# Optimization experiments

Measured on AMD Instinct MI355X. Metric: run time of the kernel, lower is better.

Reference implementation:

```python
import jax, jax.numpy as jnp
import numpy as np

N, T, M, D, H, FD, FF, L, B = 24, 120, 3, 32, 2, 16, 64, 3, 64
SCALE = 1.0 / np.sqrt(FD)  # torch MHA scales q by 1/sqrt(head_dim)
NEG = -1e9


def _make_pe():
    # Faithful to the module's (nonstandard) encoding: denominator uses 2*i/D for every i.
    t = np.arange(T, dtype=np.float64)[:, None]
    i = np.arange(D, dtype=np.float64)[None, :]
    denom = np.power(10000.0, 2.0 * i / D)
    pe = np.where(i % 2 == 0, np.sin(t / denom), np.cos(t / denom))
    return jnp.asarray(pe, jnp.float32)  # (T, D)


def _ln(x, g, b):
    mu = x.mean(-1, keepdims=True)
    var = x.var(-1, keepdims=True)
    return (x - mu) / jnp.sqrt(var + 1e-5) * g + b


def setup_inputs() -> dict:
    key = jax.random.key(0)
    keys = iter(jax.random.split(key, 48))
    def nrm(shape, s=0.1):
        return jax.random.normal(next(keys), shape, jnp.float32) * s
    inp = {
        'X': jax.random.normal(next(keys), (B, T, N * M), jnp.float32),
        'pe': _make_pe(),
        'E_W': nrm((N, M, D)), 'E_b': nrm((N, D), 0.01),
        'tq_W': nrm((N, D, D)), 'tq_b': nrm((N, D), 0.01),
        'tk_W': nrm((N, D, D)), 'tk_b': nrm((N, D), 0.01),
        'tv_W': nrm((N, D, D)), 'tv_b': nrm((N, D), 0.01),
        'tm_Wq': nrm((N, D, D)), 'tm_bq': nrm((N, D), 0.01),
        'tm_Wk': nrm((N, D, D)), 'tm_bk': nrm((N, D), 0.01),
        'tm_Wv': nrm((N, D, D)), 'tm_bv': nrm((N, D), 0.01),
        'tm_Wo': nrm((N, D, D)), 'tm_bo': nrm((N, D), 0.01),
        'sq_W': nrm((T, D, D)), 'sq_b': nrm((T, D), 0.01),
        'sk_W': nrm((T, D, D)), 'sk_b': nrm((T, D), 0.01),
        'sv_W': nrm((T, D, D)), 'sv_b': nrm((T, D), 0.01),
        'sm_Wq': nrm((T, D, D)), 'sm_bq': nrm((T, D), 0.01),
        'sm_Wk': nrm((T, D, D)), 'sm_bk': nrm((T, D), 0.01),
        'sm_Wv': nrm((T, D, D)), 'sm_bv': nrm((T, D), 0.01),
        'sm_Wo': nrm((T, D, D)), 'sm_bo': nrm((T, D), 0.01),
        'ff1_W': nrm((D, FF)), 'ff1_b': nrm((FF,), 0.01),
        'ff2_W': nrm((FF, D)), 'ff2_b': nrm((D,), 0.01),
        'ln_g': jnp.ones((D,), jnp.float32), 'ln_b': jnp.zeros((D,), jnp.float32),
        'op_W': nrm((N, D, M)), 'op_b': nrm((N, M), 0.01),
    }
    return inp


def reference(X, pe, E_W, E_b, tq_W, tq_b, tk_W, tk_b, tv_W, tv_b,
              tm_Wq, tm_bq, tm_Wk, tm_bk, tm_Wv, tm_bv, tm_Wo, tm_bo,
              sq_W, sq_b, sk_W, sk_b, sv_W, sv_b,
              sm_Wq, sm_bq, sm_Wk, sm_bk, sm_Wv, sm_bv, sm_Wo, sm_bo,
              ff1_W, ff1_b, ff2_W, ff2_b, ln_g, ln_b, op_W, op_b):
    b = X.shape[0]
    Xr = X.reshape(b, T, N, M)
    # per-joint embedding + positional encoding (dropout = identity in eval)
    E = jnp.einsum('btnm,nmd->btnd', Xr, E_W) + E_b + pe[None, :, None, :]
    causal = jnp.triu(jnp.full((T, T), NEG, jnp.float32), 1)
    for _ in range(L):
        # ---- temporal attention: per node n, causal over time ----
        q = jnp.einsum('btnd,nde->btne', E, tq_W) + tq_b
        k = jnp.einsum('btnd,nde->btne', E, tk_W) + tk_b
        v = jnp.einsum('btnd,nde->btne', E, tv_W) + tv_b
        qp = (jnp.einsum('btnd,nde->btne', q, tm_Wq) + tm_bq).reshape(b, T, N, H, FD)
        kp = (jnp.einsum('btnd,nde->btne', k, tm_Wk) + tm_bk).reshape(b, T, N, H, FD)
        vp = (jnp.einsum('btnd,nde->btne', v, tm_Wv) + tm_bv).reshape(b, T, N, H, FD)
        scores = jnp.einsum('bqnhf,bknhf->bnhqk', qp, kp) * SCALE + causal
        attn = jax.nn.softmax(scores, axis=-1)
        o = jnp.einsum('bnhqk,bknhf->bqnhf', attn, vp).reshape(b, T, N, D)
        t_sum = jnp.einsum('btnd,nde->btne', o, tm_Wo) + tm_bo
        t_norm = _ln(E + t_sum, ln_g, ln_b)
        # ---- spatial attention: per timestep t, full over nodes ----
        q = jnp.einsum('btnd,tde->btne', E, sq_W) + sq_b[:, None]
        k = jnp.einsum('btnd,tde->btne', E, sk_W) + sk_b[:, None]
        v = jnp.einsum('btnd,tde->btne', E, sv_W) + sv_b[:, None]
        qp = (jnp.einsum('btnd,tde->btne', q, sm_Wq) + sm_bq[:, None]).reshape(b, T, N, H, FD)
        kp = (jnp.einsum('btnd,tde->btne', k, sm_Wk) + sm_bk[:, None]).reshape(b, T, N, H, FD)
        vp = (jnp.einsum('btnd,tde->btne', v, sm_Wv) + sm_bv[:, None]).reshape(b, T, N, H, FD)
        scores = jnp.einsum('btqhf,btkhf->bthqk', qp, kp) * SCALE
        attn = jax.nn.softmax(scores, axis=-1)
        o = jnp.einsum('bthqk,btkhf->btqhf', attn, vp).reshape(b, T, N, D)
        s_sum = jnp.einsum('btnd,tde->btne', o, sm_Wo) + sm_bo[:, None]
        s_norm = _ln(E + s_sum, ln_g, ln_b)
        # ---- shared feedforward + norm ----
        ts = t_norm + s_norm
        ff = jax.nn.relu(ts @ ff1_W + ff1_b) @ ff2_W + ff2_b
        E = _ln(ff + ts, ln_g, ln_b)
    out = jnp.einsum('btnd,ndm->btnm', E, op_W) + op_b
    return out.reshape(b, T, N * M) + X
```

## Files before the change

kernel.cpp:

```cpp
#include <hip/hip_runtime.h>
#include <hip/hip_bf16.h>

typedef __hip_bfloat16 bf16;
typedef __fp16 h2 __attribute__((ext_vector_type(2)));
typedef _Float16 f16x2 __attribute__((ext_vector_type(2)));

constexpr int B  = 64, T = 120, N = 24, M = 3, D = 32;
constexpr int NH = 2, FD = 16, FF = 64, L = 3;
constexpr float SCALE = 0.25f;
constexpr int SK  = 40;
constexpr int SOH = 20;
constexpr int CH2 = 30;
constexpr int NJ  = 30;
constexpr int QR  = 64;
constexpr int QCH = (B * T) / QR;
constexpr int QEH = 20;
constexpr int BG  = 2;
constexpr int SR  = N * BG;
constexpr int SEH = 20;
constexpr int FR  = 32;

__device__ __forceinline__ float b2f(bf16 x) { return __bfloat162float(x); }
__device__ __forceinline__ float blo(unsigned u) { return __uint_as_float(u << 16); }
__device__ __forceinline__ float bhi(unsigned u) { return __uint_as_float(u & 0xffff0000u); }
__device__ __forceinline__ unsigned pk2(float a, float b) {
  bf16 x = __float2bfloat16(a), y = __float2bfloat16(b);
  unsigned short ux = *reinterpret_cast<unsigned short*>(&x);
  unsigned short uy = *reinterpret_cast<unsigned short*>(&y);
  return (unsigned)ux | ((unsigned)uy << 16);
}
__device__ __forceinline__ unsigned pkh2(float a, float b) {
  h2 r = __builtin_amdgcn_cvt_pkrtz(a, b);
  return *reinterpret_cast<unsigned*>(&r);
}
__device__ __forceinline__ h2 u2h(unsigned u) { return *reinterpret_cast<h2*>(&u); }
__device__ __forceinline__ f16x2 u2f(unsigned u) { return *reinterpret_cast<f16x2*>(&u); }

__global__ __launch_bounds__(256) void compose3_kernel(
    const float* __restrict__ W1q, const float* __restrict__ b1q,
    const float* __restrict__ W2q, const float* __restrict__ b2q,
    const float* __restrict__ W1k, const float* __restrict__ b1k,
    const float* __restrict__ W2k, const float* __restrict__ b2k,
    const float* __restrict__ W1v, const float* __restrict__ b1v,
    const float* __restrict__ W2v, const float* __restrict__ b2v,
    float* __restrict__ Wc, float* __restrict__ bc, int U) {
  int fam = blockIdx.x / U;
  int n   = blockIdx.x % U;
  const float* W1 = (fam == 0) ? W1q : (fam == 1) ? W1k : W1v;
  const float* b1 = (fam == 0) ? b1q : (fam == 1) ? b1k : b1v;
  const float* W2 = (fam == 0) ? W2q : (fam == 1) ? W2k : W2v;
  const float* b2 = (fam == 0) ? b2q : (fam == 1) ? b2k : b2v;
  const float* w1 = W1 + n * D * D;
  const float* w2 = W2 + n * D * D;
  float* wc  = Wc + (size_t)(fam * U + n) * D * D;
  float* bcp = bc + (fam * U + n) * D;
  __shared__ float s1[D * D], s2[D * D];
  for (int i = threadIdx.x; i < D * D; i += 256) { s1[i] = w1[i]; s2[i] = w2[i]; }
  __syncthreads();
  for (int i = threadIdx.x; i < D * D; i += 256) {
    int d = i >> 5, f = i & 31;
    float acc = 0.f;
#pragma unroll
    for (int e = 0; e < D; ++e) acc += s1[d * D + e] * s2[e * D + f];
    wc[i] = acc;
  }
  if (threadIdx.x < D) {
    int f = threadIdx.x;
    float acc = b2[n * D + f];
#pragma unroll
    for (int e = 0; e < D; ++e) acc += b1[n * D + e] * s2[e * D + f];
    bcp[f] = acc;
  }
}

__global__ __launch_bounds__(256) void embed_kernel(
    const float* __restrict__ X, const float* __restrict__ pe,
    const float* __restrict__ E_W, const float* __restrict__ E_b,
    bf16* __restrict__ E) {
  int idx = blockIdx.x * 256 + threadIdx.x;
  if (idx >= B * T * N * D) return;
  int d = idx & 31;
  int n = (idx >> 5) % N;
  int bt = idx / (D * N);
  int t = bt % T;
  const float* x = X + bt * (N * M) + n * M;
  float acc = E_b[n * D + d] + pe[t * D + d];
#pragma unroll
  for (int m = 0; m < M; ++m) acc += x[m] * E_W[(n * M + m) * D + d];
  E[idx] = __float2bfloat16(acc);
}

__global__ __launch_bounds__(256) void qkvt_kernel(
    const bf16* __restrict__ E, const float* __restrict__ WtC,
    const float* __restrict__ btC,
    bf16* __restrict__ Qt, bf16* __restrict__ Kt, bf16* __restrict__ Vt) {
  int n     = blockIdx.x / QCH;
  int chunk = blockIdx.x % QCH;
  __shared__ unsigned whh[3 * (D / 2) * D];
  __shared__ float bsh[3 * D];
  __shared__ __align__(16) unsigned Esp[QR * QEH];
  int tid = threadIdx.x;
  for (int i = tid; i < 3 * (D / 2) * D; i += 256) {
    int fam = i / ((D / 2) * D);
    int idx = i % ((D / 2) * D);
    int d2 = idx >> 5, j = idx & 31;
    const float* wg = WtC + (size_t)(fam * N + n) * D * D;
    whh[i] = pkh2(wg[(2 * d2) * D + j], wg[(2 * d2 + 1) * D + j]);
  }
  if (tid < 3 * D) {
    int fam = tid >> 5, e = tid & 31;
    bsh[tid] = btC[(fam * N + n) * D + e];
  }
  {
    int row = tid >> 2, p = tid & 3;
    const bf16* er = E + ((size_t)(chunk * QR + row) * N + n) * D;
    uint4 u = *(const uint4*)&er[p * 8];
    uint4 o;
    o.x = pkh2(blo(u.x), bhi(u.x));
    o.y = pkh2(blo(u.y), bhi(u.y));
    o.z = pkh2(blo(u.z), bhi(u.z));
    o.w = pkh2(blo(u.w), bhi(u.w));
    *(uint4*)&Esp[row * QEH + p * 4] = o;
  }
  __syncthreads();

  int row = tid >> 2, q = tid & 3;
  int grow = chunk * QR + row;
  int b = grow / T, t = grow % T;
  unsigned xp[D / 2];
#pragma unroll
  for (int d2 = 0; d2 < D / 2; ++d2) xp[d2] = Esp[row * QEH + d2];
  size_t dsto = (((size_t)b * N + n) * T + t) * D + q * 8;
  bf16* dsts[3] = { Qt + dsto, Kt + dsto, Vt + dsto };
#pragma unroll
  for (int fam = 0; fam < 3; ++fam) {
    const unsigned* wf = whh + fam * (D / 2) * D;
    const float* bi = bsh + fam * D;
    float a[8];
#pragma unroll
    for (int j = 0; j < 8; ++j) a[j] = bi[q * 8 + j];
#pragma unroll
    for (int d2 = 0; d2 < D / 2; ++d2) {
      h2 x = u2h(xp[d2]);
#pragma unroll
      for (int j = 0; j < 8; ++j)
        a[j] = __builtin_amdgcn_fdot2(x, u2h(wf[d2 * D + q * 8 + j]), a[j], false);
    }
    uint4 o;
    o.x = pk2(a[0], a[1]); o.y = pk2(a[2], a[3]);
    o.z = pk2(a[4], a[5]); o.w = pk2(a[6], a[7]);
    *(uint4*)dsts[fam] = o;
  }
}

__global__ __launch_bounds__(256) void attnt_kernel(
    const bf16* __restrict__ Qt, const bf16* __restrict__ Kt,
    const bf16* __restrict__ Vt, const bf16* __restrict__ E,
    const float* __restrict__ tm_Wo, const float* __restrict__ tm_bo,
    const float* __restrict__ ln_g, const float* __restrict__ ln_b,
    bf16* __restrict__ Tn) {
  int bn = blockIdx.x;
  int n  = bn % N, b = bn / N;
  __shared__ __align__(16) __fp16 Klh[T * SK];
  __shared__ __align__(16) __fp16 Vlh[T * SK];
  __shared__ __align__(16) __fp16 Qlh[CH2 * SK];
  __shared__ __align__(16) unsigned Olh[CH2 * SOH];
  __shared__ unsigned woh[(D / 2) * D];
  __shared__ float bol[D], gl[D], bbl[D];
  int tid = threadIdx.x;

  const bf16* Kg = Kt + (size_t)bn * T * D;
  const bf16* Vg = Vt + (size_t)bn * T * D;
  const bf16* Qg = Qt + (size_t)bn * T * D;
  for (int i = tid; i < T * 4; i += 256) {
    int r = i >> 2, p = i & 3;
    uint4 ku = *(const uint4*)&Kg[r * D + p * 8];
    uint4 kh;
    kh.x = pkh2(blo(ku.x), bhi(ku.x));
    kh.y = pkh2(blo(ku.y), bhi(ku.y));
    kh.z = pkh2(blo(ku.z), bhi(ku.z));
    kh.w = pkh2(blo(ku.w), bhi(ku.w));
    *(uint4*)&Klh[r * SK + p * 8] = kh;
    uint4 vu = *(const uint4*)&Vg[r * D + p * 8];
    uint4 vh;
    vh.x = pkh2(blo(vu.x), bhi(vu.x));
    vh.y = pkh2(blo(vu.y), bhi(vu.y));
    vh.z = pkh2(blo(vu.z), bhi(vu.z));
    vh.w = pkh2(blo(vu.w), bhi(vu.w));
    *(uint4*)&Vlh[r * SK + p * 8] = vh;
  }
  {
    const float* wg = tm_Wo + (size_t)n * D * D;
    for (int i = tid; i < (D / 2) * D; i += 256) {
      int d2 = i >> 5, e = i & 31;
      woh[i] = pkh2(wg[(2 * d2) * D + e], wg[(2 * d2 + 1) * D + e]);
    }
  }
  if (tid < D) {
    bol[tid] = tm_bo[n * D + tid];
    gl[tid]  = ln_g[tid];
    bbl[tid] = ln_b[tid];
  }
  __syncthreads();

#pragma unroll
  for (int c = 0; c < 4; ++c) {
    const int JM = (CH2 * (c + 1) + 3) >> 2;
    if (tid < CH2 * 4) {
      int r = tid >> 2, p = tid & 3;
      uint4 qu = *(const uint4*)&Qg[(CH2 * c + r) * D + p * 8];
      uint4 qh;
      qh.x = pkh2(blo(qu.x), bhi(qu.x));
      qh.y = pkh2(blo(qu.y), bhi(qu.y));
      qh.z = pkh2(blo(qu.z), bhi(qu.z));
      qh.w = pkh2(blo(qu.w), bhi(qu.w));
      *(uint4*)&Qlh[r * SK + p * 8] = qh;
    }
    __syncthreads();

    {
      int task = tid >> 2, sl = tid & 3;
      if (task < 2 * CH2) {
        int rl = task >> 1, h = task & 1, ho = h * FD;
        int rg = CH2 * c + rl;
        uint4 q0 = *(const uint4*)&Qlh[rl * SK + ho];
        uint4 q1 = *(const uint4*)&Qlh[rl * SK + ho + 8];
        unsigned qh[8] = { q0.x, q0.y, q0.z, q0.w, q1.x, q1.y, q1.z, q1.w };

        float sc[NJ];
        float mx = -3e38f;
#pragma unroll
        for (int j = 0; j < JM; ++j) {
          int k = 4 * j + sl;
          sc[j] = -3e38f;
          if (k <= rg) {
            const uint4 ka = *(const uint4*)&Klh[k * SK + ho];
            const uint4 kb = *(const uint4*)&Klh[k * SK + ho + 8];
            float s0 = __builtin_amdgcn_fdot2(u2h(qh[0]), u2h(ka.x), 0.f, false);
            float s1 = __builtin_amdgcn_fdot2(u2h(qh[1]), u2h(ka.y), 0.f, false);
            float s2 = __builtin_amdgcn_fdot2(u2h(qh[2]), u2h(ka.z), 0.f, false);
            float s3 = __builtin_amdgcn_fdot2(u2h(qh[3]), u2h(ka.w), 0.f, false);
            s0 = __builtin_amdgcn_fdot2(u2h(qh[4]), u2h(kb.x), s0, false);
            s1 = __builtin_amdgcn_fdot2(u2h(qh[5]), u2h(kb.y), s1, false);
            s2 = __builtin_amdgcn_fdot2(u2h(qh[6]), u2h(kb.z), s2, false);
            s3 = __builtin_amdgcn_fdot2(u2h(qh[7]), u2h(kb.w), s3, false);
            float s = ((s0 + s1) + (s2 + s3)) * SCALE;
            sc[j] = s;
            mx = fmaxf(mx, s);
          }
        }
        mx = fmaxf(mx, __shfl_xor(mx, 1, 64));
        mx = fmaxf(mx, __shfl_xor(mx, 2, 64));
        float l = 0.f;
#pragma unroll
        for (int j = 0; j < JM; ++j) {
          sc[j] = __expf(sc[j] - mx);
          l += sc[j];
        }
        l += __shfl_xor(l, 1, 64);
        l += __shfl_xor(l, 2, 64);
        float rli = 1.f / l;

        f16x2 acc2[8];
#pragma unroll
        for (int f = 0; f < 8; ++f) acc2[f] = f16x2{(_Float16)0.f, (_Float16)0.f};
#pragma unroll
        for (int j = 0; j < JM; ++j) {
          int k = 4 * j + sl;
          if (k <= rg) {
            f16x2 pp = f16x2{(_Float16)sc[j], (_Float16)sc[j]};
            const uint4 va = *(const uint4*)&Vlh[k * SK + ho];
            const uint4 vb = *(const uint4*)&Vlh[k * SK + ho + 8];
            acc2[0] += pp * u2f(va.x);
            acc2[1] += pp * u2f(va.y);
            acc2[2] += pp * u2f(va.z);
            acc2[3] += pp * u2f(va.w);
            acc2[4] += pp * u2f(vb.x);
            acc2[5] += pp * u2f(vb.y);
            acc2[6] += pp * u2f(vb.z);
            acc2[7] += pp * u2f(vb.w);
          }
        }
#pragma unroll
        for (int f = 0; f < 8; ++f) {
          unsigned u = *reinterpret_cast<unsigned*>(&acc2[f]);
          unsigned u1 = __shfl_xor(u, 1, 64);
          acc2[f] += u2f(u1);
          u = *reinterpret_cast<unsigned*>(&acc2[f]);
          unsigned u2_ = __shfl_xor(u, 2, 64);
          acc2[f] += u2f(u2_);
        }
        if (sl == 0) {
#pragma unroll
          for (int j = 0; j < 8; ++j)
            Olh[rl * SOH + h * 8 + j] =
                pkh2((float)acc2[j][0] * rli, (float)acc2[j][1] * rli);
        }
      }
    }
    __syncthreads();

    {
      int rl = tid >> 3, q = tid & 7, e0 = q * 4;
      if (rl < CH2) {
        int rg = CH2 * c + rl;
        size_t rowo = ((size_t)(b * T + rg) * N + n) * D;
        uint2 eu = *(const uint2*)&E[rowo + e0];
        float res[4] = { blo(eu.x), bhi(eu.x), blo(eu.y), bhi(eu.y) };
        float o[4], s1 = 0.f, s2 = 0.f;
#pragma unroll
        for (int j = 0; j < 4; ++j) {
          int e = e0 + j;
          float a = bol[e] + res[j];
#pragma unroll
          for (int d2 = 0; d2 < D / 2; ++d2)
            a = __builtin_amdgcn_fdot2(u2h(Olh[rl * SOH + d2]),
                                       u2h(woh[d2 * D + e]), a, false);
          o[j] = a; s1 += a; s2 += a * a;
        }
        s1 += __shfl_xor(s1, 1, 64); s2 += __shfl_xor(s2, 1, 64);
        s1 += __shfl_xor(s1, 2, 64); s2 += __shfl_xor(s2, 2, 64);
        s1 += __shfl_xor(s1, 4, 64); s2 += __shfl_xor(s2, 4, 64);
        float mu  = s1 * (1.f / D);
        float var = s2 * (1.f / D) - mu * mu;
        float r = rsqrtf(var + 1e-5f);
        uint2 ou;
        ou.x = pk2((o[0]-mu)*r*gl[e0]+bbl[e0],    (o[1]-mu)*r*gl[e0+1]+bbl[e0+1]);
        ou.y = pk2((o[2]-mu)*r*gl[e0+2]+bbl[e0+2],(o[3]-mu)*r*gl[e0+3]+bbl[e0+3]);
        *(uint2*)&Tn[rowo + e0] = ou;
      }
    }
  }
}

__global__ __launch_bounds__(256) void spatial_kernel(
    const bf16* __restrict__ E, const float* __restrict__ WsC,
    const float* __restrict__ bsC, const float* __restrict__ sm_Wo,
    const float* __restrict__ sm_bo, const float* __restrict__ ln_g,
    const float* __restrict__ ln_b, bf16* __restrict__ Sn) {
  int t  = blockIdx.x >> 5;
  int bg = blockIdx.x & 31;
  int b0 = bg * BG;
  __shared__ unsigned Wh[3 * (D / 2) * D];
  __shared__ unsigned woh[(D / 2) * D];
  __shared__ float bqs[D], bks[D], bvs[D], bos[D], gs[D], bbs[D];
  __shared__ __align__(16) unsigned Esh[SR * SEH];
  __shared__ __align__(16) __fp16 Qh[SR * SK];
  __shared__ __align__(16) __fp16 Kh[SR * SK];
  __shared__ __align__(16) __fp16 Vh[SR * SK];
  int tid = threadIdx.x;

  for (int i = tid; i < 3 * (D / 2) * D; i += 256) {
    int fam = i / ((D / 2) * D);
    int idx = i % ((D / 2) * D);
    int d2 = idx >> 5, e = idx & 31;
    const float* wg = WsC + (size_t)(fam * T + t) * D * D;
    Wh[i] = pkh2(wg[(2 * d2) * D + e], wg[(2 * d2 + 1) * D + e]);
  }
  {
    const float* wg = sm_Wo + (size_t)t * D * D;
    for (int i = tid; i < (D / 2) * D; i += 256) {
      int d2 = i >> 5, e = i & 31;
      woh[i] = pkh2(wg[(2 * d2) * D + e], wg[(2 * d2 + 1) * D + e]);
    }
  }
  if (tid < D) {
    bqs[tid] = bsC[(0 * T + t) * D + tid];
    bks[tid] = bsC[(1 * T + t) * D + tid];
    bvs[tid] = bsC[(2 * T + t) * D + tid];
    bos[tid] = sm_bo[t * D + tid];
    gs[tid]  = ln_g[tid];
    bbs[tid] = ln_b[tid];
  }
  if (tid < SR * 4) {
    int r = tid >> 2, p = tid & 3;
    int b = b0 + r / N, n = r % N;
    uint4 u = *(const uint4*)&E[(((size_t)b * T + t) * N + n) * D + p * 8];
    uint4 o;
    o.x = pkh2(blo(u.x), bhi(u.x));
    o.y = pkh2(blo(u.y), bhi(u.y));
    o.z = pkh2(blo(u.z), bhi(u.z));
    o.w = pkh2(blo(u.w), bhi(u.w));
    *(uint4*)&Esh[r * SEH + p * 4] = o;
  }
  __syncthreads();

#pragma unroll 1
  for (int i = tid; i < SR * D; i += 256) {
    int r = i >> 5, e = i & 31;
    float aq = bqs[e], ak = bks[e], av = bvs[e];
#pragma unroll
    for (int d2 = 0; d2 < D / 2; ++d2) {
      h2 x = u2h(Esh[r * SEH + d2]);
      aq = __builtin_amdgcn_fdot2(x, u2h(Wh[0 * 512 + d2 * 32 + e]), aq, false);
      ak = __builtin_amdgcn_fdot2(x, u2h(Wh[1 * 512 + d2 * 32 + e]), ak, false);
      av = __builtin_amdgcn_fdot2(x, u2h(Wh[2 * 512 + d2 * 32 + e]), av, false);
    }
    Qh[r * SK + e] = (__fp16)aq;
    Kh[r * SK + e] = (__fp16)ak;
    Vh[r * SK + e] = (__fp16)av;
  }
  __syncthreads();

  if (tid < SR * NH) {
    int r = tid >> 1, h = tid & 1, ho = h * FD;
    int kb = (r >= N) ? N : 0;
    uint4 q0 = *(const uint4*)&Qh[r * SK + ho];
    uint4 q1 = *(const uint4*)&Qh[r * SK + ho + 8];
    unsigned qh[8] = { q0.x, q0.y, q0.z, q0.w, q1.x, q1.y, q1.z, q1.w };
    float sc[N];
    float m = -1e30f;
#pragma unroll
    for (int k = 0; k < N; ++k) {
      const uint4 ka = *(const uint4*)&Kh[(kb + k) * SK + ho];
      const uint4 kc = *(const uint4*)&Kh[(kb + k) * SK + ho + 8];
      float s0 = __builtin_amdgcn_fdot2(u2h(qh[0]), u2h(ka.x), 0.f, false);
      float s1 = __builtin_amdgcn_fdot2(u2h(qh[1]), u2h(ka.y), 0.f, false);
      float s2 = __builtin_amdgcn_fdot2(u2h(qh[2]), u2h(ka.z), 0.f, false);
      float s3 = __builtin_amdgcn_fdot2(u2h(qh[3]), u2h(ka.w), 0.f, false);
      s0 = __builtin_amdgcn_fdot2(u2h(qh[4]), u2h(kc.x), s0, false);
      s1 = __builtin_amdgcn_fdot2(u2h(qh[5]), u2h(kc.y), s1, false);
      s2 = __builtin_amdgcn_fdot2(u2h(qh[6]), u2h(kc.z), s2, false);
      s3 = __builtin_amdgcn_fdot2(u2h(qh[7]), u2h(kc.w), s3, false);
      float s = ((s0 + s1) + (s2 + s3)) * SCALE;
      sc[k] = s;
      m = fmaxf(m, s);
    }
    float l = 0.f;
#pragma unroll
    for (int k = 0; k < N; ++k) { sc[k] = __expf(sc[k] - m); l += sc[k]; }
    float rl = 1.f / l;

    f16x2 acc2[8];
#pragma unroll
    for (int f = 0; f < 8; ++f) acc2[f] = f16x2{(_Float16)0.f, (_Float16)0.f};
#pragma unroll
    for (int k = 0; k < N; ++k) {
      f16x2 pp = f16x2{(_Float16)sc[k], (_Float16)sc[k]};
      const uint4 va = *(const uint4*)&Vh[(kb + k) * SK + ho];
      const uint4 vb = *(const uint4*)&Vh[(kb + k) * SK + ho + 8];
      acc2[0] += pp * u2f(va.x);
      acc2[1] += pp * u2f(va.y);
      acc2[2] += pp * u2f(va.z);
      acc2[3] += pp * u2f(va.w);
      acc2[4] += pp * u2f(vb.x);
      acc2[5] += pp * u2f(vb.y);
      acc2[6] += pp * u2f(vb.z);
      acc2[7] += pp * u2f(vb.w);
    }
    unsigned* op = (unsigned*)&Qh[r * SK + ho];
#pragma unroll
    for (int j = 0; j < 8; ++j)
      op[j] = pkh2((float)acc2[j][0] * rl, (float)acc2[j][1] * rl);
  }
  __syncthreads();

#pragma unroll 1
  for (int it = 0; it < 2; ++it) {
    int rl = it * 32 + (tid >> 3);
    int q = tid & 7, e0 = q * 4;
    if (rl < SR) {
      const unsigned* opk = (const unsigned*)&Qh[rl * SK];
      unsigned r0u = Esh[rl * SEH + (e0 >> 1)];
      unsigned r1u = Esh[rl * SEH + (e0 >> 1) + 1];
      h2 ra = u2h(r0u), rb = u2h(r1u);
      float res[4] = { (float)ra[0], (float)ra[1], (float)rb[0], (float)rb[1] };
      float o[4], s1 = 0.f, s2 = 0.f;
#pragma unroll
      for (int j = 0; j < 4; ++j) {
        int e = e0 + j;
        float a = bos[e] + res[j];
#pragma unroll
        for (int d2 = 0; d2 < D / 2; ++d2)
          a = __builtin_amdgcn_fdot2(u2h(opk[d2]), u2h(woh[d2 * D + e]), a, false);
        o[j] = a; s1 += a; s2 += a * a;
      }
      s1 += __shfl_xor(s1, 1, 64); s2 += __shfl_xor(s2, 1, 64);
      s1 += __shfl_xor(s1, 2, 64); s2 += __shfl_xor(s2, 2, 64);
      s1 += __shfl_xor(s1, 4, 64); s2 += __shfl_xor(s2, 4, 64);
      float mu  = s1 * (1.f / D);
      float var = s2 * (1.f / D) - mu * mu;
      float rr = rsqrtf(var + 1e-5f);
      int b = b0 + rl / N, n = rl % N;
      uint2 ou;
      ou.x = pk2((o[0]-mu)*rr*gs[e0]+bbs[e0],    (o[1]-mu)*rr*gs[e0+1]+bbs[e0+1]);
      ou.y = pk2((o[2]-mu)*rr*gs[e0+2]+bbs[e0+2],(o[3]-mu)*rr*gs[e0+3]+bbs[e0+3]);
      *(uint2*)&Sn[(((size_t)b * T + t) * N + n) * D + e0] = ou;
    }
  }
}

__global__ __launch_bounds__(256) void ff_kernel(
    const bf16* __restrict__ Tn, const bf16* __restrict__ Sn,
    const float* __restrict__ W1, const float* __restrict__ b1,
    const float* __restrict__ W2, const float* __restrict__ b2,
    const float* __restrict__ ln_g, const float* __restrict__ ln_b,
    bf16* __restrict__ E) {
  __shared__ unsigned w1h[(D / 2) * FF];
  __shared__ unsigned w2h[(FF / 2) * D];
  __shared__ float bb1[FF], bb2[D], gs[D], bbs[D];
  __shared__ unsigned tslp[FR][D / 2 + 1];
  __shared__ unsigned hlp[FR][FF / 2 + 1];
  int tid = threadIdx.x;
  int r0 = blockIdx.x * FR;
  for (int i = tid; i < (D / 2) * FF; i += 256) {
    int d2 = i / FF, jj = i % FF;
    w1h[i] = pkh2(W1[(2 * d2) * FF + jj], W1[(2 * d2 + 1) * FF + jj]);
  }
  for (int i = tid; i < (FF / 2) * D; i += 256) {
    int k2 = i / D, e = i % D;
    w2h[i] = pkh2(W2[(2 * k2) * D + e], W2[(2 * k2 + 1) * D + e]);
  }
  if (tid < FF) bb1[tid] = b1[tid];
  if (tid < D) { bb2[tid] = b2[tid]; gs[tid] = ln_g[tid]; bbs[tid] = ln_b[tid]; }
  int r = tid >> 3, s = tid & 7;
  {
    const bf16* tp = Tn + ((size_t)(r0 + r)) * D + s * 4;
    const bf16* sp = Sn + ((size_t)(r0 + r)) * D + s * 4;
    uint2 tu = *(const uint2*)tp;
    uint2 su = *(const uint2*)sp;
    float t0 = blo(tu.x) + blo(su.x);
    float t1 = bhi(tu.x) + bhi(su.x);
    float t2 = blo(tu.y) + blo(su.y);
    float t3 = bhi(tu.y) + bhi(su.y);
    tslp[r][s * 2]     = pkh2(t0, t1);
    tslp[r][s * 2 + 1] = pkh2(t2, t3);
  }
  __syncthreads();
  {
    float hh[8];
#pragma unroll
    for (int j = 0; j < 8; ++j) {
      int jj = s * 8 + j;
      float a = bb1[jj];
#pragma unroll
      for (int d2 = 0; d2 < D / 2; ++d2)
        a = __builtin_amdgcn_fdot2(u2h(tslp[r][d2]), u2h(w1h[d2 * FF + jj]), a, false);
      hh[j] = fmaxf(a, 0.f);
    }
#pragma unroll
    for (int j = 0; j < 4; ++j)
      hlp[r][s * 4 + j] = pkh2(hh[2 * j], hh[2 * j + 1]);
  }
  __syncthreads();
  {
    float x[4];
    float s1 = 0.f, s2 = 0.f;
#pragma unroll
    for (int j4 = 0; j4 < 4; ++j4) {
      int e = s * 4 + j4;
      h2 tv = u2h(tslp[r][e >> 1]);
      float a = bb2[e] + (float)tv[j4 & 1];
#pragma unroll
      for (int k2 = 0; k2 < FF / 2; ++k2)
        a = __builtin_amdgcn_fdot2(u2h(hlp[r][k2]), u2h(w2h[k2 * D + e]), a, false);
      x[j4] = a; s1 += a; s2 += a * a;
    }
    s1 += __shfl_xor(s1, 1, 64); s2 += __shfl_xor(s2, 1, 64);
    s1 += __shfl_xor(s1, 2, 64); s2 += __shfl_xor(s2, 2, 64);
    s1 += __shfl_xor(s1, 4, 64); s2 += __shfl_xor(s2, 4, 64);
    float mu  = s1 * (1.f / D);
    float var = s2 * (1.f / D) - mu * mu;
    float rr = rsqrtf(var + 1e-5f);
    int e0 = s * 4;
    uint2 ou;
    ou.x = pk2((x[0]-mu)*rr*gs[e0]+bbs[e0],    (x[1]-mu)*rr*gs[e0+1]+bbs[e0+1]);
    ou.y = pk2((x[2]-mu)*rr*gs[e0+2]+bbs[e0+2],(x[3]-mu)*rr*gs[e0+3]+bbs[e0+3]);
    *(uint2*)&E[((size_t)(r0 + r)) * D + e0] = ou;
  }
}

__global__ __launch_bounds__(256) void out_kernel(
    const bf16* __restrict__ E, const float* __restrict__ op_W,
    const float* __restrict__ op_b, const float* __restrict__ X,
    float* __restrict__ out) {
  int idx = blockIdx.x * 256 + threadIdx.x;
  if (idx >= B * T * N * M) return;
  int m  = idx % M;
  int n  = (idx / M) % N;
  int bt = idx / (M * N);
  float acc = op_b[n * M + m];
  const bf16* e = E + ((size_t)bt * N + n) * D;
#pragma unroll
  for (int d = 0; d < D; ++d) acc += b2f(e[d]) * op_W[(n * D + d) * M + m];
  acc += X[idx];
  out[idx] = acc;
}

extern "C" void kernel_launch(void* const* d_in, const int* in_sizes, int n_in,
                              void* d_out, int out_size, void* d_ws, size_t ws_size,
                              hipStream_t stream) {
  const float* X     = (const float*)d_in[0];
  const float* pe    = (const float*)d_in[1];
  const float* E_W   = (const float*)d_in[2];
  const float* E_b   = (const float*)d_in[3];
  const float* tq_W  = (const float*)d_in[4];
  const float* tq_b  = (const float*)d_in[5];
  const float* tk_W  = (const float*)d_in[6];
  const float* tk_b  = (const float*)d_in[7];
  const float* tv_W  = (const float*)d_in[8];
  const float* tv_b  = (const float*)d_in[9];
  const float* tm_Wq = (const float*)d_in[10];
  const float* tm_bq = (const float*)d_in[11];
  const float* tm_Wk = (const float*)d_in[12];
  const float* tm_bk = (const float*)d_in[13];
  const float* tm_Wv = (const float*)d_in[14];
  const float* tm_bv = (const float*)d_in[15];
  const float* tm_Wo = (const float*)d_in[16];
  const float* tm_bo = (const float*)d_in[17];
  const float* sq_W  = (const float*)d_in[18];
  const float* sq_b  = (const float*)d_in[19];
  const float* sk_W  = (const float*)d_in[20];
  const float* sk_b  = (const float*)d_in[21];
  const float* sv_W  = (const float*)d_in[22];
  const float* sv_b  = (const float*)d_in[23];
  const float* sm_Wq = (const float*)d_in[24];
  const float* sm_bq = (const float*)d_in[25];
  const float* sm_Wk = (const float*)d_in[26];
  const float* sm_bk = (const float*)d_in[27];
  const float* sm_Wv = (const float*)d_in[28];
  const float* sm_bv = (const float*)d_in[29];
  const float* sm_Wo = (const float*)d_in[30];
  const float* sm_bo = (const float*)d_in[31];
  const float* ff1_W = (const float*)d_in[32];
  const float* ff1_b = (const float*)d_in[33];
  const float* ff2_W = (const float*)d_in[34];
  const float* ff2_b = (const float*)d_in[35];
  const float* ln_g  = (const float*)d_in[36];
  const float* ln_b  = (const float*)d_in[37];
  const float* op_W  = (const float*)d_in[38];
  const float* op_b  = (const float*)d_in[39];
  float* out = (float*)d_out;

  float* WtC = (float*)d_ws;
  float* btC = WtC + 3 * N * D * D;
  float* WsC = btC + 3 * N * D;
  float* bsC = WsC + 3 * T * D * D;
  size_t act = (size_t)B * T * N * D;
  bf16* Ebuf = (bf16*)(bsC + 3 * T * D);
  bf16* Tn   = Ebuf + act;
  bf16* Qt   = Tn + act;
  bf16* Kt   = Qt + act;
  bf16* Vt   = Kt + act;
  bf16* Sn   = Qt;

  compose3_kernel<<<3 * N, 256, 0, stream>>>(
      tq_W, tq_b, tm_Wq, tm_bq, tk_W, tk_b, tm_Wk, tm_bk,
      tv_W, tv_b, tm_Wv, tm_bv, WtC, btC, N);
  compose3_kernel<<<3 * T, 256, 0, stream>>>(
      sq_W, sq_b, sm_Wq, sm_bq, sk_W, sk_b, sm_Wk, sm_bk,
      sv_W, sv_b, sm_Wv, sm_bv, WsC, bsC, T);

  embed_kernel<<<(B * T * N * D) / 256, 256, 0, stream>>>(X, pe, E_W, E_b, Ebuf);

  for (int l = 0; l < L; ++l) {
    qkvt_kernel<<<N * QCH, 256, 0, stream>>>(Ebuf, WtC, btC, Qt, Kt, Vt);
    attnt_kernel<<<B * N, 256, 0, stream>>>(Qt, Kt, Vt, Ebuf, tm_Wo, tm_bo, ln_g, ln_b, Tn);
    spatial_kernel<<<T * (B / BG), 256, 0, stream>>>(Ebuf, WsC, bsC, sm_Wo, sm_bo, ln_g, ln_b, Sn);
    ff_kernel<<<(B * T * N) / FR, 256, 0, stream>>>(Tn, Sn, ff1_W, ff1_b, ff2_W, ff2_b, ln_g, ln_b, Ebuf);
  }

  out_kernel<<<(B * T * N * M + 255) / 256, 256, 0, stream>>>(Ebuf, op_W, op_b, X, out);
}
```

Baseline: 438.0 us.

## Fuse temporal QKV projection and spatial attention into one launch

Merges the temporal QKV projection kernel and the spatial attention kernel into one launch, with blocks dispatched by index and shared memory overlaid through a union-like buffer. Spatial output gets its own workspace buffer when the workspace is large enough, so both stages can share a launch before temporal attention. This is meant to fill the GPU with independent work and drop one launch per layer. In exchange, shared memory per block becomes the larger of the two stages, which may lower occupancy for the QKV blocks, and a fallback path keeps the old ordering when the workspace is too small.

```diff
diff --git a/kernel.cpp b/kernel.cpp
--- a/kernel.cpp
+++ b/kernel.cpp
@@ -19,6 +19,8 @@
 constexpr int SR  = N * BG;
 constexpr int SEH = 20;
 constexpr int FR  = 32;
+constexpr int QG  = N * QCH;
+constexpr int SG  = T * (B / BG);
 
 __device__ __forceinline__ float b2f(bf16 x) { return __bfloat162float(x); }
 __device__ __forceinline__ float blo(unsigned u) { return __uint_as_float(u << 16); }
@@ -90,66 +92,234 @@
   E[idx] = __float2bfloat16(acc);
 }
 
-__global__ __launch_bounds__(256) void qkvt_kernel(
+struct QSmem {
+  unsigned whh[3 * (D / 2) * D];
+  float bsh[3 * D];
+  unsigned Esp[QR * QEH];
+};
+struct SSmem {
+  unsigned Wh[3 * (D / 2) * D];
+  unsigned woh[(D / 2) * D];
+  float bqs[D], bks[D], bvs[D], bos[D], gs[D], bbs[D];
+  unsigned Esh[SR * SEH];
+  __fp16 Qh[SR * SK];
+  __fp16 Kh[SR * SK];
+  __fp16 Vh[SR * SK];
+};
+constexpr size_t FUSED_SMEM =
+    sizeof(SSmem) > sizeof(QSmem) ? sizeof(SSmem) : sizeof(QSmem);
+
+__global__ __launch_bounds__(256) void qs_fused_kernel(
     const bf16* __restrict__ E, const float* __restrict__ WtC,
     const float* __restrict__ btC,
-    bf16* __restrict__ Qt, bf16* __restrict__ Kt, bf16* __restrict__ Vt) {
-  int n     = blockIdx.x / QCH;
-  int chunk = blockIdx.x % QCH;
-  __shared__ unsigned whh[3 * (D / 2) * D];
-  __shared__ float bsh[3 * D];
-  __shared__ __align__(16) unsigned Esp[QR * QEH];
+    bf16* __restrict__ Qt, bf16* __restrict__ Kt, bf16* __restrict__ Vt,
+    const float* __restrict__ WsC, const float* __restrict__ bsC,
+    const float* __restrict__ sm_Wo, const float* __restrict__ sm_bo,
+    const float* __restrict__ ln_g, const float* __restrict__ ln_b,
+    bf16* __restrict__ Sn, int qblocks) {
+  __shared__ __align__(16) char smem[FUSED_SMEM];
   int tid = threadIdx.x;
-  for (int i = tid; i < 3 * (D / 2) * D; i += 256) {
-    int fam = i / ((D / 2) * D);
-    int idx = i % ((D / 2) * D);
-    int d2 = idx >> 5, j = idx & 31;
-    const float* wg = WtC + (size_t)(fam * N + n) * D * D;
-    whh[i] = pkh2(wg[(2 * d2) * D + j], wg[(2 * d2 + 1) * D + j]);
-  }
-  if (tid < 3 * D) {
-    int fam = tid >> 5, e = tid & 31;
-    bsh[tid] = btC[(fam * N + n) * D + e];
-  }
-  {
-    int row = tid >> 2, p = tid & 3;
-    const bf16* er = E + ((size_t)(chunk * QR + row) * N + n) * D;
-    uint4 u = *(const uint4*)&er[p * 8];
-    uint4 o;
-    o.x = pkh2(blo(u.x), bhi(u.x));
-    o.y = pkh2(blo(u.y), bhi(u.y));
-    o.z = pkh2(blo(u.z), bhi(u.z));
-    o.w = pkh2(blo(u.w), bhi(u.w));
-    *(uint4*)&Esp[row * QEH + p * 4] = o;
-  }
-  __syncthreads();
-
-  int row = tid >> 2, q = tid & 3;
-  int grow = chunk * QR + row;
-  int b = grow / T, t = grow % T;
-  unsigned xp[D / 2];
-#pragma unroll
-  for (int d2 = 0; d2 < D / 2; ++d2) xp[d2] = Esp[row * QEH + d2];
-  size_t dsto = (((size_t)b * N + n) * T + t) * D + q * 8;
-  bf16* dsts[3] = { Qt + dsto, Kt + dsto, Vt + dsto };
-#pragma unroll
-  for (int fam = 0; fam < 3; ++fam) {
-    const unsigned* wf = whh + fam * (D / 2) * D;
-    const float* bi = bsh + fam * D;
-    float a[8];
-#pragma unroll
-    for (int j = 0; j < 8; ++j) a[j] = bi[q * 8 + j];
-#pragma unroll
-    for (int d2 = 0; d2 < D / 2; ++d2) {
-      h2 x = u2h(xp[d2]);
+
+  if ((int)blockIdx.x < qblocks) {
+    QSmem& q = *reinterpret_cast<QSmem*>(smem);
+    int n     = blockIdx.x / QCH;
+    int chunk = blockIdx.x % QCH;
+    for (int i = tid; i < 3 * (D / 2) * D; i += 256) {
+      int fam = i / ((D / 2) * D);
+      int idx = i % ((D / 2) * D);
+      int d2 = idx >> 5, j = idx & 31;
+      const float* wg = WtC + (size_t)(fam * N + n) * D * D;
+      q.whh[i] = pkh2(wg[(2 * d2) * D + j], wg[(2 * d2 + 1) * D + j]);
+    }
+    if (tid < 3 * D) {
+      int fam = tid >> 5, e = tid & 31;
+      q.bsh[tid] = btC[(fam * N + n) * D + e];
+    }
+    {
+      int row = tid >> 2, p = tid & 3;
+      const bf16* er = E + ((size_t)(chunk * QR + row) * N + n) * D;
+      uint4 u = *(const uint4*)&er[p * 8];
+      uint4 o;
+      o.x = pkh2(blo(u.x), bhi(u.x));
+      o.y = pkh2(blo(u.y), bhi(u.y));
+      o.z = pkh2(blo(u.z), bhi(u.z));
+      o.w = pkh2(blo(u.w), bhi(u.w));
+      *(uint4*)&q.Esp[row * QEH + p * 4] = o;
+    }
+    __syncthreads();
+
+    int row = tid >> 2, qd = tid & 3;
+    int grow = chunk * QR + row;
+    int b = grow / T, t = grow % T;
+    unsigned xp[D / 2];
+#pragma unroll
+    for (int d2 = 0; d2 < D / 2; ++d2) xp[d2] = q.Esp[row * QEH + d2];
+    size_t dsto = (((size_t)b * N + n) * T + t) * D + qd * 8;
+    bf16* dsts[3] = { Qt + dsto, Kt + dsto, Vt + dsto };
+#pragma unroll
+    for (int fam = 0; fam < 3; ++fam) {
+      const unsigned* wf = q.whh + fam * (D / 2) * D;
+      const float* bi = q.bsh + fam * D;
+      float a[8];
+#pragma unroll
+      for (int j = 0; j < 8; ++j) a[j] = bi[qd * 8 + j];
+#pragma unroll
+      for (int d2 = 0; d2 < D / 2; ++d2) {
+        h2 x = u2h(xp[d2]);
+#pragma unroll
+        for (int j = 0; j < 8; ++j)
+          a[j] = __builtin_amdgcn_fdot2(x, u2h(wf[d2 * D + qd * 8 + j]), a[j], false);
+      }
+      uint4 o;
+      o.x = pk2(a[0], a[1]); o.y = pk2(a[2], a[3]);
+      o.z = pk2(a[4], a[5]); o.w = pk2(a[6], a[7]);
+      *(uint4*)dsts[fam] = o;
+    }
+  } else {
+    SSmem& s = *reinterpret_cast<SSmem*>(smem);
+    int sb = blockIdx.x - qblocks;
+    int t  = sb >> 5;
+    int bg = sb & 31;
+    int b0 = bg * BG;
+
+    for (int i = tid; i < 3 * (D / 2) * D; i += 256) {
+      int fam = i / ((D / 2) * D);
+      int idx = i % ((D / 2) * D);
+      int d2 = idx >> 5, e = idx & 31;
+      const float* wg = WsC + (size_t)(fam * T + t) * D * D;
+      s.Wh[i] = pkh2(wg[(2 * d2) * D + e], wg[(2 * d2 + 1) * D + e]);
+    }
+    {
+      const float* wg = sm_Wo + (size_t)t * D * D;
+      for (int i = tid; i < (D / 2) * D; i += 256) {
+        int d2 = i >> 5, e = i & 31;
+        s.woh[i] = pkh2(wg[(2 * d2) * D + e], wg[(2 * d2 + 1) * D + e]);
+      }
+    }
+    if (tid < D) {
+      s.bqs[tid] = bsC[(0 * T + t) * D + tid];
+      s.bks[tid] = bsC[(1 * T + t) * D + tid];
+      s.bvs[tid] = bsC[(2 * T + t) * D + tid];
+      s.bos[tid] = sm_bo[t * D + tid];
+      s.gs[tid]  = ln_g[tid];
+      s.bbs[tid] = ln_b[tid];
+    }
+    if (tid < SR * 4) {
+      int r = tid >> 2, p = tid & 3;
+      int b = b0 + r / N, n = r % N;
+      uint4 u = *(const uint4*)&E[(((size_t)b * T + t) * N + n) * D + p * 8];
+      uint4 o;
+      o.x = pkh2(blo(u.x), bhi(u.x));
+      o.y = pkh2(blo(u.y), bhi(u.y));
+      o.z = pkh2(blo(u.z), bhi(u.z));
+      o.w = pkh2(blo(u.w), bhi(u.w));
+      *(uint4*)&s.Esh[r * SEH + p * 4] = o;
+    }
+    __syncthreads();
+
+#pragma unroll 1
+    for (int i = tid; i < SR * D; i += 256) {
+      int r = i >> 5, e = i & 31;
+      float aq = s.bqs[e], ak = s.bks[e], av = s.bvs[e];
+#pragma unroll
+      for (int d2 = 0; d2 < D / 2; ++d2) {
+        h2 x = u2h(s.Esh[r * SEH + d2]);
+        aq = __builtin_amdgcn_fdot2(x, u2h(s.Wh[0 * 512 + d2 * 32 + e]), aq, false);
+        ak = __builtin_amdgcn_fdot2(x, u2h(s.Wh[1 * 512 + d2 * 32 + e]), ak, false);
+        av = __builtin_amdgcn_fdot2(x, u2h(s.Wh[2 * 512 + d2 * 32 + e]), av, false);
+      }
+      s.Qh[r * SK + e] = (__fp16)aq;
+      s.Kh[r * SK + e] = (__fp16)ak;
+      s.Vh[r * SK + e] = (__fp16)av;
+    }
+    __syncthreads();
+
+    if (tid < SR * NH) {
+      int r = tid >> 1, h = tid & 1, ho = h * FD;
+      int kb = (r >= N) ? N : 0;
+      uint4 q0 = *(const uint4*)&s.Qh[r * SK + ho];
+      uint4 q1 = *(const uint4*)&s.Qh[r * SK + ho + 8];
+      unsigned qh[8] = { q0.x, q0.y, q0.z, q0.w, q1.x, q1.y, q1.z, q1.w };
+      float sc[N];
+      float m = -1e30f;
+#pragma unroll
+      for (int k = 0; k < N; ++k) {
+        const uint4 ka = *(const uint4*)&s.Kh[(kb + k) * SK + ho];
+        const uint4 kc = *(const uint4*)&s.Kh[(kb + k) * SK + ho + 8];
+        float s0 = __builtin_amdgcn_fdot2(u2h(qh[0]), u2h(ka.x), 0.f, false);
+        float s1 = __builtin_amdgcn_fdot2(u2h(qh[1]), u2h(ka.y), 0.f, false);
+        float s2 = __builtin_amdgcn_fdot2(u2h(qh[2]), u2h(ka.z), 0.f, false);
+        float s3 = __builtin_amdgcn_fdot2(u2h(qh[3]), u2h(ka.w), 0.f, false);
+        s0 = __builtin_amdgcn_fdot2(u2h(qh[4]), u2h(kc.x), s0, false);
+        s1 = __builtin_amdgcn_fdot2(u2h(qh[5]), u2h(kc.y), s1, false);
+        s2 = __builtin_amdgcn_fdot2(u2h(qh[6]), u2h(kc.z), s2, false);
+        s3 = __builtin_amdgcn_fdot2(u2h(qh[7]), u2h(kc.w), s3, false);
+        float sv = ((s0 + s1) + (s2 + s3)) * SCALE;
+        sc[k] = sv;
+        m = fmaxf(m, sv);
+      }
+      float l = 0.f;
+#pragma unroll
+      for (int k = 0; k < N; ++k) { sc[k] = __expf(sc[k] - m); l += sc[k]; }
+      float rl = 1.f / l;
+
+      f16x2 acc2[8];
+#pragma unroll
+      for (int f = 0; f < 8; ++f) acc2[f] = f16x2{(_Float16)0.f, (_Float16)0.f};
+#pragma unroll
+      for (int k = 0; k < N; ++k) {
+        f16x2 pp = f16x2{(_Float16)sc[k], (_Float16)sc[k]};
+        const uint4 va = *(const uint4*)&s.Vh[(kb + k) * SK + ho];
+        const uint4 vb = *(const uint4*)&s.Vh[(kb + k) * SK + ho + 8];
+        acc2[0] += pp * u2f(va.x);
+        acc2[1] += pp * u2f(va.y);
+        acc2[2] += pp * u2f(va.z);
+        acc2[3] += pp * u2f(va.w);
+        acc2[4] += pp * u2f(vb.x);
+        acc2[5] += pp * u2f(vb.y);
+        acc2[6] += pp * u2f(vb.z);
+        acc2[7] += pp * u2f(vb.w);
+      }
+      unsigned* op = (unsigned*)&s.Qh[r * SK + ho];
 #pragma unroll
       for (int j = 0; j < 8; ++j)
-        a[j] = __builtin_amdgcn_fdot2(x, u2h(wf[d2 * D + q * 8 + j]), a[j], false);
-    }
-    uint4 o;
-    o.x = pk2(a[0], a[1]); o.y = pk2(a[2], a[3]);
-    o.z = pk2(a[4], a[5]); o.w = pk2(a[6], a[7]);
-    *(uint4*)dsts[fam] = o;
+        op[j] = pkh2((float)acc2[j][0] * rl, (float)acc2[j][1] * rl);
+    }
+    __syncthreads();
+
+#pragma unroll 1
+    for (int it = 0; it < 2; ++it) {
+      int rl = it * 32 + (tid >> 3);
+      int qd = tid & 7, e0 = qd * 4;
+      if (rl < SR) {
+        const unsigned* opk = (const unsigned*)&s.Qh[rl * SK];
+        unsigned r0u = s.Esh[rl * SEH + (e0 >> 1)];
+        unsigned r1u = s.Esh[rl * SEH + (e0 >> 1) + 1];
+        h2 ra = u2h(r0u), rb = u2h(r1u);
+        float res[4] = { (float)ra[0], (float)ra[1], (float)rb[0], (float)rb[1] };
+        float o[4], s1 = 0.f, s2 = 0.f;
+#pragma unroll
+        for (int j = 0; j < 4; ++j) {
+          int e = e0 + j;
+          float a = s.bos[e] + res[j];
+#pragma unroll
+          for (int d2 = 0; d2 < D / 2; ++d2)
+            a = __builtin_amdgcn_fdot2(u2h(opk[d2]), u2h(s.woh[d2 * D + e]), a, false);
+          o[j] = a; s1 += a; s2 += a * a;
+        }
+        s1 += __shfl_xor(s1, 1, 64); s2 += __shfl_xor(s2, 1, 64);
+        s1 += __shfl_xor(s1, 2, 64); s2 += __shfl_xor(s2, 2, 64);
+        s1 += __shfl_xor(s1, 4, 64); s2 += __shfl_xor(s2, 4, 64);
+        float mu  = s1 * (1.f / D);
+        float var = s2 * (1.f / D) - mu * mu;
+        float rr = rsqrtf(var + 1e-5f);
+        int b = b0 + rl / N, n = rl % N;
+        uint2 ou;
+        ou.x = pk2((o[0]-mu)*rr*s.gs[e0]+s.bbs[e0],    (o[1]-mu)*rr*s.gs[e0+1]+s.bbs[e0+1]);
+        ou.y = pk2((o[2]-mu)*rr*s.gs[e0+2]+s.bbs[e0+2],(o[3]-mu)*rr*s.gs[e0+3]+s.bbs[e0+3]);
+        *(uint2*)&Sn[(((size_t)b * T + t) * N + n) * D + e0] = ou;
+      }
+    }
   }
 }
 
@@ -329,163 +499,6 @@
         ou.y = pk2((o[2]-mu)*r*gl[e0+2]+bbl[e0+2],(o[3]-mu)*r*gl[e0+3]+bbl[e0+3]);
         *(uint2*)&Tn[rowo + e0] = ou;
       }
-    }
-  }
-}
-
-__global__ __launch_bounds__(256) void spatial_kernel(
-    const bf16* __restrict__ E, const float* __restrict__ WsC,
-    const float* __restrict__ bsC, const float* __restrict__ sm_Wo,
-    const float* __restrict__ sm_bo, const float* __restrict__ ln_g,
-    const float* __restrict__ ln_b, bf16* __restrict__ Sn) {
-  int t  = blockIdx.x >> 5;
-  int bg = blockIdx.x & 31;
-  int b0 = bg * BG;
-  __shared__ unsigned Wh[3 * (D / 2) * D];
-  __shared__ unsigned woh[(D / 2) * D];
-  __shared__ float bqs[D], bks[D], bvs[D], bos[D], gs[D], bbs[D];
-  __shared__ __align__(16) unsigned Esh[SR * SEH];
-  __shared__ __align__(16) __fp16 Qh[SR * SK];
-  __shared__ __align__(16) __fp16 Kh[SR * SK];
-  __shared__ __align__(16) __fp16 Vh[SR * SK];
-  int tid = threadIdx.x;
-
-  for (int i = tid; i < 3 * (D / 2) * D; i += 256) {
-    int fam = i / ((D / 2) * D);
-    int idx = i % ((D / 2) * D);
-    int d2 = idx >> 5, e = idx & 31;
-    const float* wg = WsC + (size_t)(fam * T + t) * D * D;
-    Wh[i] = pkh2(wg[(2 * d2) * D + e], wg[(2 * d2 + 1) * D + e]);
-  }
-  {
-    const float* wg = sm_Wo + (size_t)t * D * D;
-    for (int i = tid; i < (D / 2) * D; i += 256) {
-      int d2 = i >> 5, e = i & 31;
-      woh[i] = pkh2(wg[(2 * d2) * D + e], wg[(2 * d2 + 1) * D + e]);
-    }
-  }
-  if (tid < D) {
-    bqs[tid] = bsC[(0 * T + t) * D + tid];
-    bks[tid] = bsC[(1 * T + t) * D + tid];
-    bvs[tid] = bsC[(2 * T + t) * D + tid];
-    bos[tid] = sm_bo[t * D + tid];
-    gs[tid]  = ln_g[tid];
-    bbs[tid] = ln_b[tid];
-  }
-  if (tid < SR * 4) {
-    int r = tid >> 2, p = tid & 3;
-    int b = b0 + r / N, n = r % N;
-    uint4 u = *(const uint4*)&E[(((size_t)b * T + t) * N + n) * D + p * 8];
-    uint4 o;
-    o.x = pkh2(blo(u.x), bhi(u.x));
-    o.y = pkh2(blo(u.y), bhi(u.y));
-    o.z = pkh2(blo(u.z), bhi(u.z));
-    o.w = pkh2(blo(u.w), bhi(u.w));
-    *(uint4*)&Esh[r * SEH + p * 4] = o;
-  }
-  __syncthreads();
-
-#pragma unroll 1
-  for (int i = tid; i < SR * D; i += 256) {
-    int r = i >> 5, e = i & 31;
-    float aq = bqs[e], ak = bks[e], av = bvs[e];
-#pragma unroll
-    for (int d2 = 0; d2 < D / 2; ++d2) {
-      h2 x = u2h(Esh[r * SEH + d2]);
-      aq = __builtin_amdgcn_fdot2(x, u2h(Wh[0 * 512 + d2 * 32 + e]), aq, false);
-      ak = __builtin_amdgcn_fdot2(x, u2h(Wh[1 * 512 + d2 * 32 + e]), ak, false);
-      av = __builtin_amdgcn_fdot2(x, u2h(Wh[2 * 512 + d2 * 32 + e]), av, false);
-    }
-    Qh[r * SK + e] = (__fp16)aq;
-    Kh[r * SK + e] = (__fp16)ak;
-    Vh[r * SK + e] = (__fp16)av;
-  }
-  __syncthreads();
-
-  if (tid < SR * NH) {
-    int r = tid >> 1, h = tid & 1, ho = h * FD;
-    int kb = (r >= N) ? N : 0;
-    uint4 q0 = *(const uint4*)&Qh[r * SK + ho];
-    uint4 q1 = *(const uint4*)&Qh[r * SK + ho + 8];
-    unsigned qh[8] = { q0.x, q0.y, q0.z, q0.w, q1.x, q1.y, q1.z, q1.w };
-    float sc[N];
-    float m = -1e30f;
-#pragma unroll
-    for (int k = 0; k < N; ++k) {
-      const uint4 ka = *(const uint4*)&Kh[(kb + k) * SK + ho];
-      const uint4 kc = *(const uint4*)&Kh[(kb + k) * SK + ho + 8];
-      float s0 = __builtin_amdgcn_fdot2(u2h(qh[0]), u2h(ka.x), 0.f, false);
-      float s1 = __builtin_amdgcn_fdot2(u2h(qh[1]), u2h(ka.y), 0.f, false);
-      float s2 = __builtin_amdgcn_fdot2(u2h(qh[2]), u2h(ka.z), 0.f, false);
-      float s3 = __builtin_amdgcn_fdot2(u2h(qh[3]), u2h(ka.w), 0.f, false);
-      s0 = __builtin_amdgcn_fdot2(u2h(qh[4]), u2h(kc.x), s0, false);
-      s1 = __builtin_amdgcn_fdot2(u2h(qh[5]), u2h(kc.y), s1, false);
-      s2 = __builtin_amdgcn_fdot2(u2h(qh[6]), u2h(kc.z), s2, false);
-      s3 = __builtin_amdgcn_fdot2(u2h(qh[7]), u2h(kc.w), s3, false);
-      float s = ((s0 + s1) + (s2 + s3)) * SCALE;
-      sc[k] = s;
-      m = fmaxf(m, s);
-    }
-    float l = 0.f;
-#pragma unroll
-    for (int k = 0; k < N; ++k) { sc[k] = __expf(sc[k] - m); l += sc[k]; }
-    float rl = 1.f / l;
-
-    f16x2 acc2[8];
-#pragma unroll
-    for (int f = 0; f < 8; ++f) acc2[f] = f16x2{(_Float16)0.f, (_Float16)0.f};
-#pragma unroll
-    for (int k = 0; k < N; ++k) {
-      f16x2 pp = f16x2{(_Float16)sc[k], (_Float16)sc[k]};
-      const uint4 va = *(const uint4*)&Vh[(kb + k) * SK + ho];
-      const uint4 vb = *(const uint4*)&Vh[(kb + k) * SK + ho + 8];
-      acc2[0] += pp * u2f(va.x);
-      acc2[1] += pp * u2f(va.y);
-      acc2[2] += pp * u2f(va.z);
-      acc2[3] += pp * u2f(va.w);
-      acc2[4] += pp * u2f(vb.x);
-      acc2[5] += pp * u2f(vb.y);
-      acc2[6] += pp * u2f(vb.z);
-      acc2[7] += pp * u2f(vb.w);
-    }
-    unsigned* op = (unsigned*)&Qh[r * SK + ho];
-#pragma unroll
-    for (int j = 0; j < 8; ++j)
-      op[j] = pkh2((float)acc2[j][0] * rl, (float)acc2[j][1] * rl);
-  }
-  __syncthreads();
-
-#pragma unroll 1
-  for (int it = 0; it < 2; ++it) {
-    int rl = it * 32 + (tid >> 3);
-    int q = tid & 7, e0 = q * 4;
-    if (rl < SR) {
-      const unsigned* opk = (const unsigned*)&Qh[rl * SK];
-      unsigned r0u = Esh[rl * SEH + (e0 >> 1)];
-      unsigned r1u = Esh[rl * SEH + (e0 >> 1) + 1];
-      h2 ra = u2h(r0u), rb = u2h(r1u);
-      float res[4] = { (float)ra[0], (float)ra[1], (float)rb[0], (float)rb[1] };
-      float o[4], s1 = 0.f, s2 = 0.f;
-#pragma unroll
-      for (int j = 0; j < 4; ++j) {
-        int e = e0 + j;
-        float a = bos[e] + res[j];
-#pragma unroll
-        for (int d2 = 0; d2 < D / 2; ++d2)
-          a = __builtin_amdgcn_fdot2(u2h(opk[d2]), u2h(woh[d2 * D + e]), a, false);
-        o[j] = a; s1 += a; s2 += a * a;
-      }
-      s1 += __shfl_xor(s1, 1, 64); s2 += __shfl_xor(s2, 1, 64);
-      s1 += __shfl_xor(s1, 2, 64); s2 += __shfl_xor(s2, 2, 64);
-      s1 += __shfl_xor(s1, 4, 64); s2 += __shfl_xor(s2, 4, 64);
-      float mu  = s1 * (1.f / D);
-      float var = s2 * (1.f / D) - mu * mu;
-      float rr = rsqrtf(var + 1e-5f);
-      int b = b0 + rl / N, n = rl % N;
-      uint2 ou;
-      ou.x = pk2((o[0]-mu)*rr*gs[e0]+bbs[e0],    (o[1]-mu)*rr*gs[e0+1]+bbs[e0+1]);
-      ou.y = pk2((o[2]-mu)*rr*gs[e0+2]+bbs[e0+2],(o[3]-mu)*rr*gs[e0+3]+bbs[e0+3]);
-      *(uint2*)&Sn[(((size_t)b * T + t) * N + n) * D + e0] = ou;
     }
   }
 }
@@ -642,7 +655,12 @@
   bf16* Qt   = Tn + act;
   bf16* Kt   = Qt + act;
   bf16* Vt   = Kt + act;
-  bf16* Sn   = Qt;
+
+  size_t floats_bytes = (size_t)(3 * N * D * D + 3 * N * D +
+                                 3 * T * D * D + 3 * T * D) * sizeof(float);
+  size_t need6 = floats_bytes + 6 * act * sizeof(bf16);
+  bool concurrent = (ws_size >= need6);
+  bf16* Sn = concurrent ? (Vt + act) : Qt;
 
   compose3_kernel<<<3 * N, 256, 0, stream>>>(
       tq_W, tq_b, tm_Wq, tm_bq, tk_W, tk_b, tm_Wk, tm_bk,
@@ -654,9 +672,20 @@
   embed_kernel<<<(B * T * N * D) / 256, 256, 0, stream>>>(X, pe, E_W, E_b, Ebuf);
 
   for (int l = 0; l < L; ++l) {
-    qkvt_kernel<<<N * QCH, 256, 0, stream>>>(Ebuf, WtC, btC, Qt, Kt, Vt);
-    attnt_kernel<<<B * N, 256, 0, stream>>>(Qt, Kt, Vt, Ebuf, tm_Wo, tm_bo, ln_g, ln_b, Tn);
-    spatial_kernel<<<T * (B / BG), 256, 0, stream>>>(Ebuf, WsC, bsC, sm_Wo, sm_bo, ln_g, ln_b, Sn);
+    if (concurrent) {
+      qs_fused_kernel<<<QG + SG, 256, 0, stream>>>(
+          Ebuf, WtC, btC, Qt, Kt, Vt,
+          WsC, bsC, sm_Wo, sm_bo, ln_g, ln_b, Sn, QG);
+      attnt_kernel<<<B * N, 256, 0, stream>>>(Qt, Kt, Vt, Ebuf, tm_Wo, tm_bo, ln_g, ln_b, Tn);
+    } else {
+      qs_fused_kernel<<<QG, 256, 0, stream>>>(
+          Ebuf, WtC, btC, Qt, Kt, Vt,
+          WsC, bsC, sm_Wo, sm_bo, ln_g, ln_b, Sn, QG);
+      attnt_kernel<<<B * N, 256, 0, stream>>>(Qt, Kt, Vt, Ebuf, tm_Wo, tm_bo, ln_g, ln_b, Tn);
+      qs_fused_kernel<<<SG, 256, 0, stream>>>(
+          Ebuf, WtC, btC, Qt, Kt, Vt,
+          WsC, bsC, sm_Wo, sm_bo, ln_g, ln_b, Sn, 0);
+    }
     ff_kernel<<<(B * T * N) / FR, 256, 0, stream>>>(Tn, Sn, ff1_W, ff1_b, ff2_W, ff2_b, ln_g, ln_b, Ebuf);
   }
 
```

Measured after the change: 422.8 us. -3.5%, faster.
